# Performance work log

Hardware: AMD Instinct MI355X
Metric: run time of the kernel (lower is better)

## Reference

```python
import jax, jax.numpy as jnp
import numpy as np

RES = 14
N = RES * RES
NH = 8
KD = 32
D = 128   # attn_ratio * key_dim
DH = 1024 # D * NH
DIM = 384
B = 128
SCALE = KD ** -0.5


def _bias_idxs():
    pts = [(i, j) for i in range(RES) for j in range(RES)]
    offs, idxs = {}, []
    for p1 in pts:
        for p2 in pts:
            o = (abs(p1[0] - p2[0]), abs(p1[1] - p2[1]))
            offs.setdefault(o, len(offs))
            idxs.append(offs[o])
    return np.array(idxs, np.int32).reshape(N, N), len(offs)

BIAS_IDXS, NUM_OFF = _bias_idxs()  # (N, N), 196 distinct |offset| pairs


def setup_inputs() -> dict:
    key = jax.random.key(0)
    ks = jax.random.split(key, 32)
    g = lambda i, shape, s=0.05: jax.random.normal(ks[i], shape, jnp.float32) * s
    pos = lambda i, shape: jax.random.uniform(ks[i], shape, jnp.float32, minval=0.5, maxval=1.5)
    return dict(
        x=jax.random.normal(ks[0], (B, DIM, RES, RES), jnp.float32),
        qw=g(1, (NH * KD, DIM)), qb=g(2, (NH * KD,)), q_s=pos(3, (NH * KD,)), q_t=g(4, (NH * KD,)),
        kw=g(5, (NH * KD, DIM)), kb=g(6, (NH * KD,)), k_s=pos(7, (NH * KD,)), k_t=g(8, (NH * KD,)),
        vw=g(9, (DH, DIM)), vb=g(10, (DH,)), v_s=pos(11, (DH,)), v_t=g(12, (DH,)),
        lvw=g(13, (DH, 3, 3)), lvb=g(14, (DH,)), lv_s=pos(15, (DH,)), lv_t=g(16, (DH,)),
        th1w=g(17, (NH, NH), 0.3), th1b=g(18, (NH,)),
        th2w=g(19, (NH, NH), 0.3), th2b=g(20, (NH,)),
        ab=g(21, (NH, NUM_OFF)),
        pw=g(22, (DIM, DH)), pb=g(23, (DIM,)), p_s=pos(24, (DIM,)), p_t=g(25, (DIM,)),
    )


def _c(v):
    return v[None, :, None, None]


def conv1x1_bn(x, w, b, s, t):
    # 1x1 conv (NCHW) + eval-mode BN folded to per-channel affine
    y = jnp.einsum('bchw,oc->bohw', x, w) + _c(b)
    return y * _c(s) + _c(t)


def reference(x, qw, qb, q_s, q_t, kw, kb, k_s, k_t, vw, vb, v_s, v_t,
              lvw, lvb, lv_s, lv_t, th1w, th1b, th2w, th2b, ab,
              pw, pb, p_s, p_t):
    Bb = x.shape[0]
    # q,k: (B, NH, N, KD)
    q = conv1x1_bn(x, qw, qb, q_s, q_t).reshape(Bb, NH, KD, N).transpose(0, 1, 3, 2)
    k = conv1x1_bn(x, kw, kb, k_s, k_t).reshape(Bb, NH, KD, N).transpose(0, 1, 3, 2)
    v4 = conv1x1_bn(x, vw, vb, v_s, v_t)  # (B, DH, RES, RES)
    # local depthwise 3x3 conv + BN on v
    vl = jax.lax.conv_general_dilated(
        v4, lvw.reshape(DH, 1, 3, 3), window_strides=(1, 1), padding='SAME',
        dimension_numbers=('NCHW', 'OIHW', 'NCHW'), feature_group_count=DH)
    vl = (vl + _c(lvb)) * _c(lv_s) + _c(lv_t)
    v = v4.reshape(Bb, NH, D, N).transpose(0, 1, 3, 2)  # (B, NH, N, D)

    attn = jnp.einsum('bhid,bhjd->bhij', q, k) * SCALE
    attn = attn + ab[:, BIAS_IDXS][None]  # relative-position bias (1, NH, N, N)
    attn = jnp.einsum('bhij,gh->bgij', attn, th1w) + _c(th1b)  # talking head 1
    attn = jax.nn.softmax(attn, axis=-1)
    attn = jnp.einsum('bhij,gh->bgij', attn, th2w) + _c(th2b)  # talking head 2

    o = jnp.einsum('bhij,bhjd->bhid', attn, v)  # (B, NH, N, D)
    o = o.transpose(0, 1, 3, 2).reshape(Bb, DH, RES, RES) + vl
    o = jax.nn.relu(o)
    return conv1x1_bn(o, pw, pb, p_s, p_t)
```

## Files before the change

### kernel.cpp

```cpp
#include <hip/hip_runtime.h>
#include <hip/hip_bf16.h>
#include <stdint.h>

typedef __hip_bfloat16 bf16;
typedef short short8 __attribute__((ext_vector_type(8)));
typedef float f32x4 __attribute__((ext_vector_type(4)));

#define NB 128
#define NPIX 196
#define NPAD 208
#define VP 224
#define QROWS 208
#define NH 8
#define KD 32
#define DHEAD 128
#define DH 1024
#define DIM 384
#define SCALE 0.17677669529663687f

__device__ __forceinline__ float b2f(bf16 v) { return __bfloat162float(v); }
__device__ __forceinline__ bf16 f2b(float f) { return __float2bfloat16(f); }
__device__ __forceinline__ float us2f(unsigned short u) {
  union { unsigned int i; float f; } v; v.i = (unsigned int)u << 16; return v.f;
}
__device__ __forceinline__ short f2us(float f) {
  bf16 b = __float2bfloat16(f);
  return *(short*)&b;
}

__device__ __forceinline__ void gll16(const void* g, void* l) {
  auto gp = reinterpret_cast<const uint32_t __attribute__((address_space(1)))*>(
      reinterpret_cast<uintptr_t>(g));
  auto lp = reinterpret_cast<uint32_t __attribute__((address_space(3)))*>(
      reinterpret_cast<uintptr_t>(l));
  __builtin_amdgcn_global_load_lds(gp, lp, 16, 0, 0);
}

__global__ __launch_bounds__(256) void k_cvt4(const float* __restrict__ s0,
                                              const float* __restrict__ s1,
                                              const float* __restrict__ s2,
                                              const float* __restrict__ s3,
                                              bf16* __restrict__ dst) {
  int i = blockIdx.x * 256 + threadIdx.x;
  if (i >= 983040) return;
  const float* src; int o;
  if (i < 98304)       { src = s0; o = i; }
  else if (i < 196608) { src = s1; o = i - 98304; }
  else if (i < 589824) { src = s2; o = i - 196608; }
  else                 { src = s3; o = i - 589824; }
  dst[i] = f2b(src[o]);
}

__global__ __launch_bounds__(256) void k_xt(const float* __restrict__ x,
                                            bf16* __restrict__ XT) {
  __shared__ bf16 tile[32][33];
  int ct = blockIdx.x, nt = blockIdx.y, b = blockIdx.z;
  int c0 = ct * 32, n0 = nt * 32;
  int tc = threadIdx.x >> 5, tn = threadIdx.x & 31;
#pragma unroll
  for (int r = 0; r < 4; ++r) {
    int c = tc + r * 8;
    int n = n0 + tn;
    float v = 0.f;
    if (n < NPIX) v = x[((size_t)b * DIM + c0 + c) * NPIX + n];
    tile[c][tn] = f2b(v);
  }
  __syncthreads();
#pragma unroll
  for (int r = 0; r < 4; ++r) {
    int n = n0 + tc + r * 8;
    if (n < NPAD) XT[((size_t)b * NPAD + n) * DIM + c0 + tn] = tile[tn][tc + r * 8];
  }
}

__global__ __launch_bounds__(256, 2) void k_qkv2(
    const bf16* __restrict__ Wf, const bf16* __restrict__ XT,
    const float* __restrict__ qb, const float* __restrict__ qs, const float* __restrict__ qt,
    const float* __restrict__ kb, const float* __restrict__ ks, const float* __restrict__ kt,
    const float* __restrict__ vb, const float* __restrict__ vs, const float* __restrict__ vt,
    bf16* __restrict__ qf, bf16* __restrict__ kf, bf16* __restrict__ v4) {
  __shared__ __align__(16) char lds[2][32768];
  const int NWG = 12 * 208;
  int id = blockIdx.x;
  int id2 = (id & 7) * (NWG >> 3) + (id >> 3);
  int mt = id2 % 12, nt = id2 / 12;
  int m0 = mt * 128, n0 = nt * 128;
  int tid = threadIdx.x, lane = tid & 63;
  int wv = tid >> 6, wm = wv >> 1, wn = wv & 1;

  f32x4 acc[4][4];
#pragma unroll
  for (int mi = 0; mi < 4; ++mi)
#pragma unroll
    for (int ni = 0; ni < 4; ++ni)
#pragma unroll
      for (int r = 0; r < 4; ++r) acc[mi][ni][r] = 0.f;

  auto stage = [&](int buf, int t) {
    int k0 = t * 64;
#pragma unroll
    for (int j = 0; j < 4; ++j) {
      int gi = tid + j * 256;
      int row = gi >> 3, g = gi & 7;
      int sk = k0 + ((g ^ (row & 7)) << 3);
      gll16(Wf + (size_t)(m0 + row) * DIM + sk, &lds[buf][gi * 16]);
      gll16(XT + (size_t)(n0 + row) * DIM + sk, &lds[buf][16384 + gi * 16]);
    }
  };
  auto compute = [&](int buf) {
    const char* Ab = lds[buf];
    const char* Bb = lds[buf] + 16384;
    int kq = lane >> 4, il = lane & 15;
#pragma unroll
    for (int ksb = 0; ksb < 2; ++ksb) {
      int G = ksb * 4 + kq;
      short8 af[4], bfr[4];
#pragma unroll
      for (int mi = 0; mi < 4; ++mi) {
        int row = wm * 64 + mi * 16 + il;
        af[mi] = *(const short8*)(Ab + row * 128 + ((G ^ (row & 7)) << 4));
      }
#pragma unroll
      for (int ni = 0; ni < 4; ++ni) {
        int row = wn * 64 + ni * 16 + il;
        bfr[ni] = *(const short8*)(Bb + row * 128 + ((G ^ (row & 7)) << 4));
      }
#pragma unroll
      for (int mi = 0; mi < 4; ++mi)
#pragma unroll
        for (int ni = 0; ni < 4; ++ni)
          acc[mi][ni] = __builtin_amdgcn_mfma_f32_16x16x32_bf16(af[mi], bfr[ni], acc[mi][ni], 0, 0, 0);
    }
  };

  stage(0, 0);
  __syncthreads();
  for (int t = 0; t < 6; ++t) {
    if (t < 5) stage((t + 1) & 1, t + 1);
    compute(t & 1);
    __syncthreads();
  }

  int cq = lane >> 4, cn = lane & 15;
#pragma unroll
  for (int mi = 0; mi < 4; ++mi) {
    int mbase = m0 + wm * 64 + mi * 16;
    const float *bp, *sp, *tp;
    int segbase, segid;
    if (mbase < 256)      { bp = qb; sp = qs; tp = qt; segbase = 0;   segid = 0; }
    else if (mbase < 512) { bp = kb; sp = ks; tp = kt; segbase = 256; segid = 1; }
    else                  { bp = vb; sp = vs; tp = vt; segbase = 512; segid = 2; }
#pragma unroll
    for (int r = 0; r < 4; ++r) {
      int ms = mbase - segbase + cq * 4 + r;
      float bi = bp[ms], sc = sp[ms], tt = tp[ms];
#pragma unroll
      for (int ni = 0; ni < 4; ++ni) {
        int n = n0 + wn * 64 + ni * 16 + cn;
        int b = n / NPAD;
        int nn = n - b * NPAD;
        float y = (acc[mi][ni][r] + bi) * sc + tt;
        y = (nn < NPIX) ? y : 0.f;
        if (segid == 2) {
          v4[((size_t)b * DH + ms) * VP + nn] = f2b(y);
        } else {
          bf16* dst = segid ? kf : qf;
          dst[(((size_t)b * NH + (ms >> 5)) * QROWS + nn) * KD + (ms & 31)] = f2b(y);
        }
      }
    }
  }
}

__global__ __launch_bounds__(256) void k_vpad(bf16* __restrict__ v4) {
  int i = blockIdx.x * 256 + threadIdx.x;
  int tot = NB * DH * 16;
  if (i < tot) {
    int row = i >> 4, c = i & 15;
    v4[(size_t)row * VP + 208 + c] = f2b(0.f);
  }
}

__global__ __launch_bounds__(256, 2) void k_p2(
    const bf16* __restrict__ Pw, const bf16* __restrict__ OT,
    const float* __restrict__ pb, const float* __restrict__ ps, const float* __restrict__ pt,
    float* __restrict__ out) {
  __shared__ __align__(16) char lds[2][32768];
  const int NWG = 3 * 208;
  int id = blockIdx.x;
  int id2 = (id & 7) * (NWG >> 3) + (id >> 3);
  int mt = id2 % 3, nt = id2 / 3;
  int m0 = mt * 128, n0 = nt * 128;
  int tid = threadIdx.x, lane = tid & 63;
  int wv = tid >> 6, wm = wv >> 1, wn = wv & 1;

  f32x4 acc[4][4];
#pragma unroll
  for (int mi = 0; mi < 4; ++mi)
#pragma unroll
    for (int ni = 0; ni < 4; ++ni)
#pragma unroll
      for (int r = 0; r < 4; ++r) acc[mi][ni][r] = 0.f;

  auto stage = [&](int buf, int t) {
    int k0 = t * 64;
#pragma unroll
    for (int j = 0; j < 4; ++j) {
      int gi = tid + j * 256;
      int row = gi >> 3, g = gi & 7;
      int sk = k0 + ((g ^ (row & 7)) << 3);
      gll16(Pw + (size_t)(m0 + row) * DH + sk, &lds[buf][gi * 16]);
      gll16(OT + (size_t)(n0 + row) * DH + sk, &lds[buf][16384 + gi * 16]);
    }
  };
  auto compute = [&](int buf) {
    const char* Ab = lds[buf];
    const char* Bb = lds[buf] + 16384;
    int kq = lane >> 4, il = lane & 15;
#pragma unroll
    for (int ksb = 0; ksb < 2; ++ksb) {
      int G = ksb * 4 + kq;
      short8 af[4], bfr[4];
#pragma unroll
      for (int mi = 0; mi < 4; ++mi) {
        int row = wm * 64 + mi * 16 + il;
        af[mi] = *(const short8*)(Ab + row * 128 + ((G ^ (row & 7)) << 4));
      }
#pragma unroll
      for (int ni = 0; ni < 4; ++ni) {
        int row = wn * 64 + ni * 16 + il;
        bfr[ni] = *(const short8*)(Bb + row * 128 + ((G ^ (row & 7)) << 4));
      }
#pragma unroll
      for (int mi = 0; mi < 4; ++mi)
#pragma unroll
        for (int ni = 0; ni < 4; ++ni)
          acc[mi][ni] = __builtin_amdgcn_mfma_f32_16x16x32_bf16(af[mi], bfr[ni], acc[mi][ni], 0, 0, 0);
    }
  };

  stage(0, 0);
  __syncthreads();
  for (int t = 0; t < 16; ++t) {
    if (t < 15) stage((t + 1) & 1, t + 1);
    compute(t & 1);
    __syncthreads();
  }

  int cq = lane >> 4, cn = lane & 15;
#pragma unroll
  for (int mi = 0; mi < 4; ++mi) {
#pragma unroll
    for (int r = 0; r < 4; ++r) {
      int m = m0 + wm * 64 + mi * 16 + cq * 4 + r;
      float bi = pb[m], sc = ps[m], tt = pt[m];
#pragma unroll
      for (int ni = 0; ni < 4; ++ni) {
        int n = n0 + wn * 64 + ni * 16 + cn;
        int b = n / NPAD;
        int nn = n - b * NPAD;
        if (nn < NPIX)
          out[((size_t)b * DIM + m) * NPIX + nn] = (acc[mi][ni][r] + bi) * sc + tt;
      }
    }
  }
}

__global__ __launch_bounds__(256) void k_dwv(
    const bf16* __restrict__ v4, const float* __restrict__ lvw,
    const float* __restrict__ lvb, const float* __restrict__ lvs,
    const float* __restrict__ lvt, bf16* __restrict__ vl,
    float* __restrict__ vcs) {
  int blk = blockIdx.x;
  int b = blk >> 8, cg = blk & 255;
  int lc = threadIdx.x >> 6, px = threadIdx.x & 63;
  int ch = cg * 4 + lc;
  const bf16* src = v4 + ((size_t)b * DH + ch) * VP;
  float w[9];
#pragma unroll
  for (int i = 0; i < 9; ++i) w[i] = lvw[ch * 9 + i];
  float bb = lvb[ch], ss = lvs[ch], tt = lvt[ch];
  bf16* dst = vl + ((size_t)b * DH + ch) * NPIX;
  float csum = 0.f;
  for (int p = px; p < NPIX; p += 64) {
    int ri = p / 14, ci = p - ri * 14;
    float s = 0.f;
#pragma unroll
    for (int dy = -1; dy <= 1; ++dy)
#pragma unroll
      for (int dx = -1; dx <= 1; ++dx) {
        int rr = ri + dy, cc = ci + dx;
        if (rr >= 0 && rr < 14 && cc >= 0 && cc < 14)
          s += w[(dy + 1) * 3 + dx + 1] * b2f(src[rr * 14 + cc]);
      }
    csum += b2f(src[p]);
    dst[p] = f2b((s + bb) * ss + tt);
  }
  csum += __shfl_xor(csum, 1);
  csum += __shfl_xor(csum, 2);
  csum += __shfl_xor(csum, 4);
  csum += __shfl_xor(csum, 8);
  csum += __shfl_xor(csum, 16);
  csum += __shfl_xor(csum, 32);
  if (px == 0) vcs[b * DH + ch] = csum;
}

#define SROW 448
__device__ __forceinline__ int saddr(int g, int i, int j) {
  int r = j * 2 + ((i & 7) << 4);
  if (r >= SROW) r -= SROW;
  return (g * 16 + i) * SROW + r;
}

__global__ __launch_bounds__(512, 2) void k_att(
    const bf16* __restrict__ qf, const bf16* __restrict__ kf,
    const bf16* __restrict__ v4, const bf16* __restrict__ vl,
    const float* __restrict__ vcs,
    const float* __restrict__ th1w, const float* __restrict__ th1b,
    const float* __restrict__ th2w, const float* __restrict__ th2b,
    const float* __restrict__ ab, bf16* __restrict__ OT) {
  __shared__ __align__(16) char smem[NH * 16 * SROW];
  __shared__ float ab2[NH * NPIX];
  __shared__ float c2s[64];
  int id = blockIdx.x;
  int xcd = id & 7;
  int rest = id >> 3;
  int qt = rest % 13;
  int b = (rest / 13) * 8 + xcd;
  int i0 = qt * 16;
  int tid = threadIdx.x;
  int wave = tid >> 6, lane = tid & 63;
  int il = lane & 15, kh = lane >> 4;

  if (tid < 64) c2s[tid] = th2w[tid];
  for (int pos = tid; pos < NH * NPIX; pos += 512) {
    int g = pos / NPIX, off = pos - g * NPIX;
    float s = th1b[g];
#pragma unroll
    for (int h = 0; h < 8; ++h)
      s += th1w[g * 8 + h] * ab[h * NPIX + off];
    ab2[pos] = s;
  }
  __syncthreads();
  {
    const bf16* qpb = qf + (size_t)b * NH * QROWS * KD + (size_t)(i0 + il) * KD + kh * 8;
    const bf16* kpb = kf + (size_t)b * NH * QROWS * KD + (size_t)il * KD + kh * 8;
    short8 qfr[8];
#pragma unroll
    for (int h = 0; h < 8; ++h) {
      short8 raw = *(const short8*)(qpb + (size_t)h * QROWS * KD);
      float c = th1w[wave * 8 + h] * SCALE;
      short8 s;
#pragma unroll
      for (int e = 0; e < 8; ++e) s[e] = f2us(us2f((unsigned short)raw[e]) * c);
      qfr[h] = s;
    }
    int ri4[4], ci4[4];
#pragma unroll
    for (int r = 0; r < 4; ++r) {
      int ia = i0 + kh * 4 + r; if (ia > 195) ia = 195;
      int rr = (ia * 4682) >> 16;
      ri4[r] = rr; ci4[r] = ia - rr * 14;
    }
    for (int jt = 0; jt < 13; ++jt) {
      f32x4 a0 = {0.f, 0.f, 0.f, 0.f};
      f32x4 a1 = {0.f, 0.f, 0.f, 0.f};
#pragma unroll
      for (int h = 0; h < 8; h += 2) {
        short8 b0 = *(const short8*)(kpb + (size_t)h * QROWS * KD + jt * 16 * KD);
        short8 b1 = *(const short8*)(kpb + (size_t)(h + 1) * QROWS * KD + jt * 16 * KD);
        a0 = __builtin_amdgcn_mfma_f32_16x16x32_bf16(qfr[h], b0, a0, 0, 0, 0);
        a1 = __builtin_amdgcn_mfma_f32_16x16x32_bf16(qfr[h + 1], b1, a1, 0, 0, 0);
      }
      int j = jt * 16 + il;
      int rj = (j * 4682) >> 16;
      int cj = j - rj * 14;
#pragma unroll
      for (int r = 0; r < 4; ++r) {
        int dr = ri4[r] > rj ? ri4[r] - rj : rj - ri4[r];
        int dc = ci4[r] > cj ? ci4[r] - cj : cj - ci4[r];
        int off = (j < NPIX) ? dr * 14 + dc : 0;
        float v = a0[r] + a1[r] + ab2[wave * NPIX + off];
        *(bf16*)(smem + saddr(wave, kh * 4 + r, j)) = f2b(v);
      }
    }
  }
  __syncthreads();
  {
    int row = tid >> 2, part = tid & 3;
    int g = row >> 4, i = row & 15;
    int jb = part * 49, je = jb + 49;
    float m = -1e30f;
    for (int j = jb; j < je; ++j)
      m = fmaxf(m, b2f(*(const bf16*)(smem + saddr(g, i, j))));
    m = fmaxf(m, __shfl_xor(m, 1));
    m = fmaxf(m, __shfl_xor(m, 2));
    float s = 0.f;
    for (int j = jb; j < je; ++j)
      s += __expf(b2f(*(const bf16*)(smem + saddr(g, i, j))) - m);
    s += __shfl_xor(s, 1);
    s += __shfl_xor(s, 2);
    float inv = 1.f / s;
    for (int j = jb; j < je; ++j) {
      bf16* p = (bf16*)(smem + saddr(g, i, j));
      *p = f2b(__expf(b2f(*p) - m) * inv);
    }
    if (part == 3)
      for (int j = NPIX; j < VP; ++j)
        *(bf16*)(smem + saddr(g, i, j)) = f2b(0.f);
  }
  __syncthreads();
  for (int pos = tid; pos < 16 * NPIX; pos += 512) {
    int i = pos / NPIX, j = pos - i * NPIX;
    float pv[8];
#pragma unroll
    for (int g = 0; g < 8; ++g) pv[g] = b2f(*(const bf16*)(smem + saddr(g, i, j)));
#pragma unroll
    for (int g2 = 0; g2 < 8; ++g2) {
      float s = 0.f;
#pragma unroll
      for (int g = 0; g < 8; ++g) s += c2s[g2 * 8 + g] * pv[g];
      *(bf16*)(smem + saddr(g2, i, j)) = f2b(s);
    }
  }
  __syncthreads();
  {
    int g = wave;
    f32x4 oacc[8];
#pragma unroll
    for (int dt = 0; dt < 8; ++dt)
#pragma unroll
      for (int r = 0; r < 4; ++r) oacc[dt][r] = 0.f;
    const bf16* vbase = v4 + ((size_t)b * DH + g * DHEAD) * VP;
    for (int ks = 0; ks < 7; ++ks) {
      short8 pa = *(const short8*)(smem + saddr(g, il, ks * 32 + kh * 8));
#pragma unroll
      for (int dt = 0; dt < 8; ++dt) {
        short8 bv = *(const short8*)(vbase + (size_t)(dt * 16 + il) * VP + ks * 32 + kh * 8);
        oacc[dt] = __builtin_amdgcn_mfma_f32_16x16x32_bf16(pa, bv, oacc[dt], 0, 0, 0);
      }
    }
    float t2b = th2b[g];
#pragma unroll
    for (int dt = 0; dt < 8; ++dt) {
      int ch = g * DHEAD + dt * 16 + il;
      float csv = vcs[b * DH + ch] * t2b;
#pragma unroll
      for (int r = 0; r < 4; ++r) {
        int n = i0 + kh * 4 + r;
        if (n < NPIX) {
          float val = oacc[dt][r] + csv + b2f(vl[((size_t)b * DH + ch) * NPIX + n]);
          OT[((size_t)b * NPAD + n) * DH + ch] = f2b(fmaxf(val, 0.f));
        } else {
          OT[((size_t)b * NPAD + n) * DH + ch] = f2b(0.f);
        }
      }
    }
  }
}

extern "C" void kernel_launch(void* const* d_in, const int* in_sizes, int n_in,
                              void* d_out, int out_size, void* d_ws, size_t ws_size,
                              hipStream_t stream) {
  const float* x    = (const float*)d_in[0];
  const float* qw   = (const float*)d_in[1];
  const float* qb   = (const float*)d_in[2];
  const float* q_s  = (const float*)d_in[3];
  const float* q_t  = (const float*)d_in[4];
  const float* kw   = (const float*)d_in[5];
  const float* kb   = (const float*)d_in[6];
  const float* k_s  = (const float*)d_in[7];
  const float* k_t  = (const float*)d_in[8];
  const float* vw   = (const float*)d_in[9];
  const float* vb   = (const float*)d_in[10];
  const float* v_s  = (const float*)d_in[11];
  const float* v_t  = (const float*)d_in[12];
  const float* lvw  = (const float*)d_in[13];
  const float* lvb  = (const float*)d_in[14];
  const float* lv_s = (const float*)d_in[15];
  const float* lv_t = (const float*)d_in[16];
  const float* th1w = (const float*)d_in[17];
  const float* th1b = (const float*)d_in[18];
  const float* th2w = (const float*)d_in[19];
  const float* th2b = (const float*)d_in[20];
  const float* ab   = (const float*)d_in[21];
  const float* pw   = (const float*)d_in[22];
  const float* pb   = (const float*)d_in[23];
  const float* p_s  = (const float*)d_in[24];
  const float* p_t  = (const float*)d_in[25];

  char* ws = (char*)d_ws;
  size_t off = 0;
  auto alloc = [&](size_t bytes) {
    char* p = ws + off;
    off += (bytes + 255) & ~(size_t)255;
    return p;
  };
  char* region0 = alloc((size_t)NB * NPAD * DH * 2);
  bf16* XT  = (bf16*)region0;
  bf16* OT  = (bf16*)region0;
  bf16* qfb = (bf16*)alloc((size_t)NB * NH * QROWS * KD * 2);
  bf16* kfb = (bf16*)alloc((size_t)NB * NH * QROWS * KD * 2);
  bf16* v4  = (bf16*)alloc((size_t)NB * DH * VP * 2);
  bf16* vlb = (bf16*)alloc((size_t)NB * DH * NPIX * 2);
  float* vcs = (float*)alloc((size_t)NB * DH * 4);
  bf16* wf  = (bf16*)alloc((size_t)1536 * DIM * 2);
  bf16* wpb = (bf16*)alloc((size_t)DIM * DH * 2);
  (void)ws_size; (void)in_sizes; (void)n_in; (void)out_size;

  k_cvt4<<<dim3(3840), 256, 0, stream>>>(qw, kw, vw, pw, wf);
  k_xt<<<dim3(12, 7, NB), 256, 0, stream>>>(x, XT);
  k_qkv2<<<dim3(2496), 256, 0, stream>>>(wf, XT, qb, q_s, q_t, kb, k_s, k_t,
                                         vb, v_s, v_t, qfb, kfb, v4);
  k_vpad<<<dim3((NB * DH * 16 + 255) / 256), 256, 0, stream>>>(v4);
  k_dwv<<<dim3(NB * 256), 256, 0, stream>>>(v4, lvw, lvb, lv_s, lv_t, vlb, vcs);
  k_att<<<dim3(1664), 512, 0, stream>>>(qfb, kfb, v4, vlb, vcs,
                                        th1w, th1b, th2w, th2b, ab, OT);
  k_p2<<<dim3(624), 256, 0, stream>>>(wpb, OT, pb, p_s, p_t, (float*)d_out);
}
```

Measured before the change: 493.3 us.

## Compute per-head QK once, apply talking-head-1 mix in shared memory, vectorize softmax

The QK stage now does a single MFMA per tile for each wave's own head, instead of eight MFMAs over all heads with a pre-scaled Q. The talking-head-1 mixing and the relative-position bias move into a separate shared-memory pass that reads all 8 head scores per element and writes the mixed values back. Softmax now reads and writes 4 bf16 values at a time and writes unnormalized exponentials. The 1/sum factor is stored per row and folded into the talking-head-2 pass, which removes one exp pass. This cuts MFMA and global K loads by about 8x, at the cost of an extra barrier and an extra LDS round trip with bf16 rounding of the raw scores.

```diff
diff --git a/kernel.cpp b/kernel.cpp
--- a/kernel.cpp
+++ b/kernel.cpp
@@ -3,6 +3,7 @@
 #include <stdint.h>
 
 typedef __hip_bfloat16 bf16;
+typedef short short4v __attribute__((ext_vector_type(4)));
 typedef short short8 __attribute__((ext_vector_type(8)));
 typedef float f32x4 __attribute__((ext_vector_type(4)));
 
@@ -321,7 +322,9 @@
     const float* __restrict__ ab, bf16* __restrict__ OT) {
   __shared__ __align__(16) char smem[NH * 16 * SROW];
   __shared__ float ab2[NH * NPIX];
+  __shared__ float c1s[64];
   __shared__ float c2s[64];
+  __shared__ float smInv[NH * 16];
   int id = blockIdx.x;
   int xcd = id & 7;
   int rest = id >> 3;
@@ -332,7 +335,10 @@
   int wave = tid >> 6, lane = tid & 63;
   int il = lane & 15, kh = lane >> 4;
 
-  if (tid < 64) c2s[tid] = th2w[tid];
+  if (tid < 64) {
+    c1s[tid] = th1w[tid] * SCALE;
+    c2s[tid] = th2w[tid];
+  }
   for (int pos = tid; pos < NH * NPIX; pos += 512) {
     int g = pos / NPIX, off = pos - g * NPIX;
     float s = th1b[g];
@@ -341,80 +347,88 @@
       s += th1w[g * 8 + h] * ab[h * NPIX + off];
     ab2[pos] = s;
   }
-  __syncthreads();
   {
-    const bf16* qpb = qf + (size_t)b * NH * QROWS * KD + (size_t)(i0 + il) * KD + kh * 8;
-    const bf16* kpb = kf + (size_t)b * NH * QROWS * KD + (size_t)il * KD + kh * 8;
-    short8 qfr[8];
-#pragma unroll
-    for (int h = 0; h < 8; ++h) {
-      short8 raw = *(const short8*)(qpb + (size_t)h * QROWS * KD);
-      float c = th1w[wave * 8 + h] * SCALE;
-      short8 s;
-#pragma unroll
-      for (int e = 0; e < 8; ++e) s[e] = f2us(us2f((unsigned short)raw[e]) * c);
-      qfr[h] = s;
-    }
-    int ri4[4], ci4[4];
-#pragma unroll
-    for (int r = 0; r < 4; ++r) {
-      int ia = i0 + kh * 4 + r; if (ia > 195) ia = 195;
-      int rr = (ia * 4682) >> 16;
-      ri4[r] = rr; ci4[r] = ia - rr * 14;
-    }
+    const bf16* qp = qf + ((size_t)b * NH + wave) * QROWS * KD;
+    const bf16* kp = kf + ((size_t)b * NH + wave) * QROWS * KD;
+    short8 a = *(const short8*)(qp + (i0 + il) * KD + kh * 8);
     for (int jt = 0; jt < 13; ++jt) {
-      f32x4 a0 = {0.f, 0.f, 0.f, 0.f};
-      f32x4 a1 = {0.f, 0.f, 0.f, 0.f};
-#pragma unroll
-      for (int h = 0; h < 8; h += 2) {
-        short8 b0 = *(const short8*)(kpb + (size_t)h * QROWS * KD + jt * 16 * KD);
-        short8 b1 = *(const short8*)(kpb + (size_t)(h + 1) * QROWS * KD + jt * 16 * KD);
-        a0 = __builtin_amdgcn_mfma_f32_16x16x32_bf16(qfr[h], b0, a0, 0, 0, 0);
-        a1 = __builtin_amdgcn_mfma_f32_16x16x32_bf16(qfr[h + 1], b1, a1, 0, 0, 0);
-      }
+      short8 bb = *(const short8*)(kp + (jt * 16 + il) * KD + kh * 8);
+      f32x4 acc = {0.f, 0.f, 0.f, 0.f};
+      acc = __builtin_amdgcn_mfma_f32_16x16x32_bf16(a, bb, acc, 0, 0, 0);
       int j = jt * 16 + il;
-      int rj = (j * 4682) >> 16;
-      int cj = j - rj * 14;
-#pragma unroll
-      for (int r = 0; r < 4; ++r) {
-        int dr = ri4[r] > rj ? ri4[r] - rj : rj - ri4[r];
-        int dc = ci4[r] > cj ? ci4[r] - cj : cj - ci4[r];
-        int off = (j < NPIX) ? dr * 14 + dc : 0;
-        float v = a0[r] + a1[r] + ab2[wave * NPIX + off];
-        *(bf16*)(smem + saddr(wave, kh * 4 + r, j)) = f2b(v);
-      }
-    }
+#pragma unroll
+      for (int r = 0; r < 4; ++r)
+        *(bf16*)(smem + saddr(wave, kh * 4 + r, j)) = f2b(acc[r]);
+    }
+  }
+  __syncthreads();
+  for (int pos = tid; pos < 16 * NPIX; pos += 512) {
+    int i = pos / NPIX, j = pos - i * NPIX;
+    float sv[8];
+#pragma unroll
+    for (int h = 0; h < 8; ++h) sv[h] = b2f(*(const bf16*)(smem + saddr(h, i, j)));
+    int ia = i0 + i; if (ia > 195) ia = 195;
+    int ri = ia / 14, ci = ia - ri * 14;
+    int rj = j / 14, cj = j - rj * 14;
+    int dr = ri > rj ? ri - rj : rj - ri;
+    int dc = ci > cj ? ci - cj : cj - ci;
+    int off = dr * 14 + dc;
+    float outv[8];
+#pragma unroll
+    for (int g = 0; g < 8; ++g) {
+      float s = ab2[g * NPIX + off];
+#pragma unroll
+      for (int h = 0; h < 8; ++h) s += c1s[g * 8 + h] * sv[h];
+      outv[g] = s;
+    }
+#pragma unroll
+    for (int g = 0; g < 8; ++g)
+      *(bf16*)(smem + saddr(g, i, j)) = f2b(outv[g]);
   }
   __syncthreads();
   {
     int row = tid >> 2, part = tid & 3;
     int g = row >> 4, i = row & 15;
-    int jb = part * 49, je = jb + 49;
+    int jb = part * 52;
+    int n4 = (part == 3) ? 10 : 13;
     float m = -1e30f;
-    for (int j = jb; j < je; ++j)
-      m = fmaxf(m, b2f(*(const bf16*)(smem + saddr(g, i, j))));
+    for (int it = 0; it < n4; ++it) {
+      short4v v = *(const short4v*)(smem + saddr(g, i, jb + it * 4));
+#pragma unroll
+      for (int t = 0; t < 4; ++t) m = fmaxf(m, us2f((unsigned short)v[t]));
+    }
     m = fmaxf(m, __shfl_xor(m, 1));
     m = fmaxf(m, __shfl_xor(m, 2));
     float s = 0.f;
-    for (int j = jb; j < je; ++j)
-      s += __expf(b2f(*(const bf16*)(smem + saddr(g, i, j))) - m);
+    for (int it = 0; it < n4; ++it) {
+      char* p = smem + saddr(g, i, jb + it * 4);
+      short4v v = *(const short4v*)p;
+      short4v w;
+#pragma unroll
+      for (int t = 0; t < 4; ++t) {
+        float e = __expf(us2f((unsigned short)v[t]) - m);
+        s += e;
+        w[t] = f2us(e);
+      }
+      *(short4v*)p = w;
+    }
+    if (part == 3) {
+      short4v z = {0, 0, 0, 0};
+#pragma unroll
+      for (int it = 0; it < 7; ++it)
+        *(short4v*)(smem + saddr(g, i, 196 + it * 4)) = z;
+    }
     s += __shfl_xor(s, 1);
     s += __shfl_xor(s, 2);
-    float inv = 1.f / s;
-    for (int j = jb; j < je; ++j) {
-      bf16* p = (bf16*)(smem + saddr(g, i, j));
-      *p = f2b(__expf(b2f(*p) - m) * inv);
-    }
-    if (part == 3)
-      for (int j = NPIX; j < VP; ++j)
-        *(bf16*)(smem + saddr(g, i, j)) = f2b(0.f);
+    if (part == 0) smInv[row] = 1.f / s;
   }
   __syncthreads();
   for (int pos = tid; pos < 16 * NPIX; pos += 512) {
     int i = pos / NPIX, j = pos - i * NPIX;
     float pv[8];
 #pragma unroll
-    for (int g = 0; g < 8; ++g) pv[g] = b2f(*(const bf16*)(smem + saddr(g, i, j)));
+    for (int g = 0; g < 8; ++g)
+      pv[g] = b2f(*(const bf16*)(smem + saddr(g, i, j))) * smInv[g * 16 + i];
 #pragma unroll
     for (int g2 = 0; g2 < 8; ++g2) {
       float s = 0.f;
```

Result: faster. 437.1 us (-11.4%).
